# Performance work log

Hardware: AMD Instinct MI355X
Metric: run time of the kernel (lower is better)

Reference implementation:

```python
import jax, jax.numpy as jnp
import numpy as np

USER_COUNT = 100000
ITEM_COUNT = 50000
N_NODES = USER_COUNT + ITEM_COUNT
NNZ = 4800000
EMB = 64
BATCH = 4096


def setup_inputs() -> dict:
    key = jax.random.key(0)
    k1, k2, k3, k4, k5, k6, k7 = jax.random.split(key, 7)
    return {
        "user_emb": jax.random.normal(k1, (USER_COUNT, EMB), dtype=jnp.float32),
        "item_emb": jax.random.normal(k2, (ITEM_COUNT, EMB), dtype=jnp.float32),
        "adj_vals": jax.random.uniform(k3, (NNZ,), dtype=jnp.float32),
        "adj_row": jax.random.randint(k4, (NNZ,), 0, N_NODES, dtype=jnp.int64),
        "adj_col": jax.random.randint(k5, (NNZ,), 0, N_NODES, dtype=jnp.int64),
        "users": jax.random.randint(k6, (BATCH,), 0, USER_COUNT, dtype=jnp.int64),
        "items": jax.random.randint(k7, (BATCH,), 0, ITEM_COUNT, dtype=jnp.int64),
        "n_layers": 3,
    }


def _spmm(adj_row, adj_col, adj_vals, x):
    # sparse (N,N) @ dense (N,D): gather source rows, scale by edge values, scatter-add to dest
    msgs = adj_vals[:, None] * x[adj_col]  # [nnz, D]
    return jax.ops.segment_sum(msgs, adj_row, num_segments=N_NODES)


def reference(user_emb, item_emb, adj_vals, adj_row, adj_col, users, items, n_layers):
    ego = jnp.concatenate([user_emb, item_emb], axis=0)  # [N, D]
    for _ in range(n_layers):
        ego = _spmm(adj_row, adj_col, adj_vals, ego)
    user_all = ego[:USER_COUNT]
    item_all = ego[USER_COUNT:]
    return (user_all[users], item_all[items])
```

## Files before the change

### kernel.cpp

```cpp
#include <hip/hip_runtime.h>
#include <hip/hip_bf16.h>

#define USER_COUNT 100000
#define ITEM_COUNT 50000
#define N_NODES    150000
#define EMB        64
#define BATCH      4096

#define NFINE      586
#define FSHIFT     8
#define NBLK_P     512
#define PTHREADS   512

__device__ inline unsigned short f2bf_raw(float f) {
    __hip_bfloat16 h = __float2bfloat16(f);
    unsigned short u; __builtin_memcpy(&u, &h, 2); return u;
}

__global__ __launch_bounds__(PTHREADS) void count_kernel(
        const int* __restrict__ rows, int* __restrict__ counts, int nnz) {
    __shared__ int cnt[NFINE];
    const int b = blockIdx.x, t = threadIdx.x;
    for (int f = t; f < NFINE; f += PTHREADS) cnt[f] = 0;
    __syncthreads();
    const int per = (nnz + NBLK_P - 1) / NBLK_P;
    const int s = b * per, e = min(s + per, nnz);
    for (int i = s + t; i < e; i += PTHREADS)
        atomicAdd(&cnt[rows[i] >> FSHIFT], 1);
    __syncthreads();
    for (int f = t; f < NFINE; f += PTHREADS)
        counts[f * NBLK_P + b] = cnt[f];
}

__global__ __launch_bounds__(NBLK_P) void reduce_tot(
        const int* __restrict__ counts, int* __restrict__ tot) {
    __shared__ int red[NBLK_P];
    const int f = blockIdx.x, t = threadIdx.x;
    red[t] = counts[f * NBLK_P + t];
    __syncthreads();
    for (int o = NBLK_P / 2; o > 0; o >>= 1) {
        if (t < o) red[t] += red[t + o];
        __syncthreads();
    }
    if (t == 0) tot[f] = red[0];
}

__global__ void scan_fbase_kernel(const int* __restrict__ tot,
                                  int* __restrict__ fbase) {
    if (threadIdx.x == 0) {
        int acc = 0;
        for (int f = 0; f < NFINE; ++f) { fbase[f] = acc; acc += tot[f]; }
    }
}

__global__ __launch_bounds__(NBLK_P) void scan_offs(
        const int* __restrict__ counts, const int* __restrict__ fbase,
        int* __restrict__ offs) {
    __shared__ int s[NBLK_P];
    const int f = blockIdx.x, t = threadIdx.x;
    const int c = counts[f * NBLK_P + t];
    s[t] = c;
    __syncthreads();
    for (int o = 1; o < NBLK_P; o <<= 1) {
        int v = (t >= o) ? s[t - o] : 0;
        __syncthreads();
        s[t] += v;
        __syncthreads();
    }
    offs[f * NBLK_P + t] = fbase[f] + s[t] - c;
}

__global__ __launch_bounds__(PTHREADS) void partition_kernel(
        const float* __restrict__ vals,
        const int* __restrict__ rows,
        const int* __restrict__ cols,
        const int* __restrict__ offs,
        uint2* __restrict__ fine, int nnz) {
    __shared__ int cur[NFINE];
    const int b = blockIdx.x, t = threadIdx.x;
    for (int f = t; f < NFINE; f += PTHREADS) cur[f] = offs[f * NBLK_P + b];
    __syncthreads();
    const int per = (nnz + NBLK_P - 1) / NBLK_P;
    const int s = b * per, e = min(s + per, nnz);
    for (int i = s + t; i < e; i += PTHREADS) {
        int r = rows[i];
        int f = r >> FSHIFT;
        int pos = atomicAdd(&cur[f], 1);
        fine[pos] = make_uint2(__float_as_uint(vals[i]),
                               (unsigned)cols[i] | ((unsigned)(r & 255) << 18));
    }
}

__global__ __launch_bounds__(256) void bucket_sort_kernel(
        const uint2* __restrict__ fine,
        const int* __restrict__ tot,
        const int* __restrict__ fbase,
        float2* __restrict__ perm,
        int* __restrict__ row_ptr) {
    __shared__ int hist[256];
    __shared__ int off[256];
    __shared__ int cur[256];
    const int f   = blockIdx.x;
    const int tid = threadIdx.x;
    const int n   = tot[f];
    const int fb  = fbase[f];
    const uint2* src = fine + fb;

    hist[tid] = 0;
    __syncthreads();
    for (int k = tid; k < n; k += 256)
        atomicAdd(&hist[(src[k].y >> 18) & 255], 1);
    __syncthreads();
    if (tid == 0) {
        int acc = 0;
        for (int j = 0; j < 256; ++j) { off[j] = acc; acc += hist[j]; }
    }
    __syncthreads();
    cur[tid] = off[tid];
    int row = (f << FSHIFT) + tid;
    if (row <= N_NODES) row_ptr[row] = fb + off[tid];
    __syncthreads();
    for (int k = tid; k < n; k += 256) {
        uint2 e = src[k];
        int lrow = (e.y >> 18) & 255;
        int pos = fb + atomicAdd(&cur[lrow], 1);
        perm[pos] = make_float2(__uint_as_float(e.x),
                                __int_as_float((int)(e.y & 0x3FFFFu)));
    }
}

__global__ void to_bf16(const float4* __restrict__ ue,
                        const float4* __restrict__ ie,
                        uint2* __restrict__ xh) {
    int i = blockIdx.x * blockDim.x + threadIdx.x;
    const int n4 = (N_NODES * EMB) / 4;
    const int u4 = (USER_COUNT * EMB) / 4;
    if (i >= n4) return;
    float4 fv = (i < u4) ? ue[i] : ie[i - u4];
    uint2 o;
    o.x = (unsigned int)f2bf_raw(fv.x) | ((unsigned int)f2bf_raw(fv.y) << 16);
    o.y = (unsigned int)f2bf_raw(fv.z) | ((unsigned int)f2bf_raw(fv.w) << 16);
    xh[i] = o;
}

__global__ void spmm_bf16(const int* __restrict__ row_ptr,
                          const float2* __restrict__ perm,
                          const unsigned short* __restrict__ xh,
                          unsigned short* __restrict__ yh) {
    int wid  = (blockIdx.x * blockDim.x + threadIdx.x) >> 6;
    int lane = threadIdx.x & 63;
    int g    = lane >> 4;
    int s    = lane & 15;
    int r    = (wid << 2) + g;
    if (r >= N_NODES) return;

    int beg = row_ptr[r];
    int end = row_ptr[r + 1];

    const uint2* xv = (const uint2*)xh;
    float ax = 0.f, ay = 0.f, az = 0.f, aw = 0.f;

    int j = beg;
    for (; j + 3 < end; j += 4) {
        float2 e0 = perm[j];
        float2 e1 = perm[j + 1];
        float2 e2 = perm[j + 2];
        float2 e3 = perm[j + 3];
        uint2 u0 = xv[(((long long)__float_as_int(e0.y)) << 4) + s];
        uint2 u1 = xv[(((long long)__float_as_int(e1.y)) << 4) + s];
        uint2 u2 = xv[(((long long)__float_as_int(e2.y)) << 4) + s];
        uint2 u3 = xv[(((long long)__float_as_int(e3.y)) << 4) + s];
        ax += e0.x * __uint_as_float(u0.x << 16);
        ay += e0.x * __uint_as_float(u0.x & 0xffff0000u);
        az += e0.x * __uint_as_float(u0.y << 16);
        aw += e0.x * __uint_as_float(u0.y & 0xffff0000u);
        ax += e1.x * __uint_as_float(u1.x << 16);
        ay += e1.x * __uint_as_float(u1.x & 0xffff0000u);
        az += e1.x * __uint_as_float(u1.y << 16);
        aw += e1.x * __uint_as_float(u1.y & 0xffff0000u);
        ax += e2.x * __uint_as_float(u2.x << 16);
        ay += e2.x * __uint_as_float(u2.x & 0xffff0000u);
        az += e2.x * __uint_as_float(u2.y << 16);
        aw += e2.x * __uint_as_float(u2.y & 0xffff0000u);
        ax += e3.x * __uint_as_float(u3.x << 16);
        ay += e3.x * __uint_as_float(u3.x & 0xffff0000u);
        az += e3.x * __uint_as_float(u3.y << 16);
        aw += e3.x * __uint_as_float(u3.y & 0xffff0000u);
    }
    for (; j < end; ++j) {
        float2 e = perm[j];
        uint2 u = xv[(((long long)__float_as_int(e.y)) << 4) + s];
        ax += e.x * __uint_as_float(u.x << 16);
        ay += e.x * __uint_as_float(u.x & 0xffff0000u);
        az += e.x * __uint_as_float(u.y << 16);
        aw += e.x * __uint_as_float(u.y & 0xffff0000u);
    }

    uint2 o;
    o.x = (unsigned int)f2bf_raw(ax) | ((unsigned int)f2bf_raw(ay) << 16);
    o.y = (unsigned int)f2bf_raw(az) | ((unsigned int)f2bf_raw(aw) << 16);
    ((uint2*)yh)[(((long long)r) << 4) + s] = o;
}

__global__ void spmm_batch_kernel(const int* __restrict__ row_ptr,
                                  const float2* __restrict__ perm,
                                  const unsigned short* __restrict__ xh,
                                  const int* __restrict__ users,
                                  const int* __restrict__ items,
                                  float4* __restrict__ out) {
    int wid  = (blockIdx.x * blockDim.x + threadIdx.x) >> 6;
    int lane = threadIdx.x & 63;
    int g    = lane >> 4;
    int s    = lane & 15;
    int b    = (wid << 2) + g;
    if (b >= 2 * BATCH) return;
    int node = (b < BATCH) ? users[b] : (USER_COUNT + items[b - BATCH]);

    int beg = row_ptr[node];
    int end = row_ptr[node + 1];

    const uint2* xv = (const uint2*)xh;
    float ax = 0.f, ay = 0.f, az = 0.f, aw = 0.f;

    int j = beg;
    for (; j + 3 < end; j += 4) {
        float2 e0 = perm[j];
        float2 e1 = perm[j + 1];
        float2 e2 = perm[j + 2];
        float2 e3 = perm[j + 3];
        uint2 u0 = xv[(((long long)__float_as_int(e0.y)) << 4) + s];
        uint2 u1 = xv[(((long long)__float_as_int(e1.y)) << 4) + s];
        uint2 u2 = xv[(((long long)__float_as_int(e2.y)) << 4) + s];
        uint2 u3 = xv[(((long long)__float_as_int(e3.y)) << 4) + s];
        ax += e0.x * __uint_as_float(u0.x << 16);
        ay += e0.x * __uint_as_float(u0.x & 0xffff0000u);
        az += e0.x * __uint_as_float(u0.y << 16);
        aw += e0.x * __uint_as_float(u0.y & 0xffff0000u);
        ax += e1.x * __uint_as_float(u1.x << 16);
        ay += e1.x * __uint_as_float(u1.x & 0xffff0000u);
        az += e1.x * __uint_as_float(u1.y << 16);
        aw += e1.x * __uint_as_float(u1.y & 0xffff0000u);
        ax += e2.x * __uint_as_float(u2.x << 16);
        ay += e2.x * __uint_as_float(u2.x & 0xffff0000u);
        az += e2.x * __uint_as_float(u2.y << 16);
        aw += e2.x * __uint_as_float(u2.y & 0xffff0000u);
        ax += e3.x * __uint_as_float(u3.x << 16);
        ay += e3.x * __uint_as_float(u3.x & 0xffff0000u);
        az += e3.x * __uint_as_float(u3.y << 16);
        aw += e3.x * __uint_as_float(u3.y & 0xffff0000u);
    }
    for (; j < end; ++j) {
        float2 e = perm[j];
        uint2 u = xv[(((long long)__float_as_int(e.y)) << 4) + s];
        ax += e.x * __uint_as_float(u.x << 16);
        ay += e.x * __uint_as_float(u.x & 0xffff0000u);
        az += e.x * __uint_as_float(u.y << 16);
        aw += e.x * __uint_as_float(u.y & 0xffff0000u);
    }

    out[(size_t)b * 16 + s] = make_float4(ax, ay, az, aw);
}

extern "C" void kernel_launch(void* const* d_in, const int* in_sizes, int n_in,
                              void* d_out, int out_size, void* d_ws, size_t ws_size,
                              hipStream_t stream) {
    const float* user_emb = (const float*)d_in[0];
    const float* item_emb = (const float*)d_in[1];
    const float* adj_vals = (const float*)d_in[2];
    const int*   adj_row  = (const int*)d_in[3];
    const int*   adj_col  = (const int*)d_in[4];
    const int*   users    = (const int*)d_in[5];
    const int*   items    = (const int*)d_in[6];

    const int nnz = in_sizes[2];

    char* p = (char*)d_ws;
    uint2* fine = (uint2*)p;
    unsigned short* xh_a = (unsigned short*)p;
    unsigned short* xh_b = xh_a + (size_t)N_NODES * EMB;
    p += (size_t)nnz * sizeof(uint2);
    float2* perm = (float2*)p;
    p += (size_t)nnz * sizeof(float2);
    int* row_ptr = (int*)p;
    p += (size_t)(N_NODES + 16) * sizeof(int);
    int* counts = (int*)p;  p += (size_t)NFINE * NBLK_P * sizeof(int);
    int* offs   = (int*)p;  p += (size_t)NFINE * NBLK_P * sizeof(int);
    int* tot    = (int*)p;  p += (size_t)NFINE * sizeof(int);
    int* fbase  = (int*)p;

    count_kernel<<<NBLK_P, PTHREADS, 0, stream>>>(adj_row, counts, nnz);
    reduce_tot<<<NFINE, NBLK_P, 0, stream>>>(counts, tot);
    scan_fbase_kernel<<<1, 64, 0, stream>>>(tot, fbase);
    scan_offs<<<NFINE, NBLK_P, 0, stream>>>(counts, fbase, offs);
    partition_kernel<<<NBLK_P, PTHREADS, 0, stream>>>(adj_vals, adj_row, adj_col,
                                                      offs, fine, nnz);
    bucket_sort_kernel<<<NFINE, 256, 0, stream>>>(fine, tot, fbase, perm, row_ptr);

    const int n4 = (N_NODES * EMB) / 4;
    to_bf16<<<(n4 + 255) / 256, 256, 0, stream>>>((const float4*)user_emb,
                                                  (const float4*)item_emb,
                                                  (uint2*)xh_a);

    const int spmm_blocks = (N_NODES / 4 + 3) / 4;
    spmm_bf16<<<spmm_blocks, 256, 0, stream>>>(row_ptr, perm, xh_a, xh_b);
    spmm_bf16<<<spmm_blocks, 256, 0, stream>>>(row_ptr, perm, xh_b, xh_a);
    spmm_batch_kernel<<<(2 * BATCH / 4 + 3) / 4, 256, 0, stream>>>(
        row_ptr, perm, xh_a, users, items, (float4*)d_out);
}
```

Measured before the change: 504.7 us.

## Stage partition tiles in LDS and widen SpMM gathers to 16-byte loads

The partition kernel now works on fixed 6400-edge tiles. It counts and scans the buckets locally, scatters edges into a shared-memory buffer, then writes each bucket's run contiguously to global memory, replacing scattered global writes. The SpMM and batch kernels assign 8 lanes per row with uint4 loads instead of 16 lanes with uint2, so one wavefront handles 8 rows and issues fewer, wider gathers. The cost is a second pass over rows, a binary search per element, heavy LDS use per block, and more registers per lane.

```diff
diff --git a/kernel.cpp b/kernel.cpp
--- a/kernel.cpp
+++ b/kernel.cpp
@@ -9,36 +9,35 @@
 
 #define NFINE      586
 #define FSHIFT     8
-#define NBLK_P     512
-#define PTHREADS   512
+#define TILE_E     6400
+#define NBSTRIDE   768
 
 __device__ inline unsigned short f2bf_raw(float f) {
     __hip_bfloat16 h = __float2bfloat16(f);
     unsigned short u; __builtin_memcpy(&u, &h, 2); return u;
 }
 
-__global__ __launch_bounds__(PTHREADS) void count_kernel(
+__global__ __launch_bounds__(512) void count_kernel(
         const int* __restrict__ rows, int* __restrict__ counts, int nnz) {
     __shared__ int cnt[NFINE];
     const int b = blockIdx.x, t = threadIdx.x;
-    for (int f = t; f < NFINE; f += PTHREADS) cnt[f] = 0;
-    __syncthreads();
-    const int per = (nnz + NBLK_P - 1) / NBLK_P;
-    const int s = b * per, e = min(s + per, nnz);
-    for (int i = s + t; i < e; i += PTHREADS)
+    for (int f = t; f < NFINE; f += 512) cnt[f] = 0;
+    __syncthreads();
+    const int s = b * TILE_E, e = min(s + TILE_E, nnz);
+    for (int i = s + t; i < e; i += 512)
         atomicAdd(&cnt[rows[i] >> FSHIFT], 1);
     __syncthreads();
-    for (int f = t; f < NFINE; f += PTHREADS)
-        counts[f * NBLK_P + b] = cnt[f];
-}
-
-__global__ __launch_bounds__(NBLK_P) void reduce_tot(
-        const int* __restrict__ counts, int* __restrict__ tot) {
-    __shared__ int red[NBLK_P];
+    for (int f = t; f < NFINE; f += 512)
+        counts[f * NBSTRIDE + b] = cnt[f];
+}
+
+__global__ __launch_bounds__(1024) void reduce_tot(
+        const int* __restrict__ counts, int* __restrict__ tot, int nblk) {
+    __shared__ int red[1024];
     const int f = blockIdx.x, t = threadIdx.x;
-    red[t] = counts[f * NBLK_P + t];
-    __syncthreads();
-    for (int o = NBLK_P / 2; o > 0; o >>= 1) {
+    red[t] = (t < nblk) ? counts[f * NBSTRIDE + t] : 0;
+    __syncthreads();
+    for (int o = 512; o > 0; o >>= 1) {
         if (t < o) red[t] += red[t + o];
         __syncthreads();
     }
@@ -53,41 +52,78 @@
     }
 }
 
-__global__ __launch_bounds__(NBLK_P) void scan_offs(
+__global__ __launch_bounds__(1024) void scan_offs(
         const int* __restrict__ counts, const int* __restrict__ fbase,
-        int* __restrict__ offs) {
-    __shared__ int s[NBLK_P];
+        int* __restrict__ offs, int nblk) {
+    __shared__ int s[1024];
     const int f = blockIdx.x, t = threadIdx.x;
-    const int c = counts[f * NBLK_P + t];
+    const int c = (t < nblk) ? counts[f * NBSTRIDE + t] : 0;
     s[t] = c;
     __syncthreads();
-    for (int o = 1; o < NBLK_P; o <<= 1) {
+    for (int o = 1; o < 1024; o <<= 1) {
         int v = (t >= o) ? s[t - o] : 0;
         __syncthreads();
         s[t] += v;
         __syncthreads();
     }
-    offs[f * NBLK_P + t] = fbase[f] + s[t] - c;
-}
-
-__global__ __launch_bounds__(PTHREADS) void partition_kernel(
+    if (t < nblk) offs[f * NBSTRIDE + t] = fbase[f] + s[t] - c;
+}
+
+__global__ __launch_bounds__(512) void partition_kernel(
         const float* __restrict__ vals,
         const int* __restrict__ rows,
         const int* __restrict__ cols,
         const int* __restrict__ offs,
         uint2* __restrict__ fine, int nnz) {
-    __shared__ int cur[NFINE];
+    __shared__ uint2 buf[TILE_E];
+    __shared__ int   cnt[NFINE];
+    __shared__ int   sloff[NFINE + 1];
+    __shared__ int   gb[NFINE];
+    __shared__ int   sscan[512];
     const int b = blockIdx.x, t = threadIdx.x;
-    for (int f = t; f < NFINE; f += PTHREADS) cur[f] = offs[f * NBLK_P + b];
-    __syncthreads();
-    const int per = (nnz + NBLK_P - 1) / NBLK_P;
-    const int s = b * per, e = min(s + per, nnz);
-    for (int i = s + t; i < e; i += PTHREADS) {
+    const int sbeg = b * TILE_E, send = min(sbeg + TILE_E, nnz);
+    const int n = send - sbeg;
+
+    for (int f = t; f < NFINE; f += 512) {
+        cnt[f] = 0;
+        gb[f] = offs[f * NBSTRIDE + b];
+    }
+    __syncthreads();
+    for (int i = sbeg + t; i < send; i += 512)
+        atomicAdd(&cnt[rows[i] >> FSHIFT], 1);
+    __syncthreads();
+    int c0 = (2 * t < NFINE) ? cnt[2 * t] : 0;
+    int c1 = (2 * t + 1 < NFINE) ? cnt[2 * t + 1] : 0;
+    sscan[t] = c0 + c1;
+    __syncthreads();
+    for (int o = 1; o < 512; o <<= 1) {
+        int v = (t >= o) ? sscan[t - o] : 0;
+        __syncthreads();
+        sscan[t] += v;
+        __syncthreads();
+    }
+    int base = (t == 0) ? 0 : sscan[t - 1];
+    if (2 * t < NFINE) sloff[2 * t] = base;
+    if (2 * t + 1 < NFINE) sloff[2 * t + 1] = base + c0;
+    if (t == 511) sloff[NFINE] = sscan[511];
+    __syncthreads();
+    for (int f = t; f < NFINE; f += 512) cnt[f] = sloff[f];
+    __syncthreads();
+    for (int i = sbeg + t; i < send; i += 512) {
         int r = rows[i];
         int f = r >> FSHIFT;
-        int pos = atomicAdd(&cur[f], 1);
-        fine[pos] = make_uint2(__float_as_uint(vals[i]),
-                               (unsigned)cols[i] | ((unsigned)(r & 255) << 18));
+        int pos = atomicAdd(&cnt[f], 1);
+        buf[pos] = make_uint2(__float_as_uint(vals[i]),
+                              (unsigned)cols[i] | ((unsigned)(r & 255) << 18));
+    }
+    __syncthreads();
+    for (int idx = t; idx < n; idx += 512) {
+        int lo = 0, hi = NFINE;
+        while (hi - lo > 1) {
+            int mid = (lo + hi) >> 1;
+            if (sloff[mid] <= idx) lo = mid; else hi = mid;
+        }
+        fine[gb[lo] + (idx - sloff[lo])] = buf[idx];
     }
 }
 
@@ -143,22 +179,33 @@
     xh[i] = o;
 }
 
+#define ACC8(U, W)                                      \
+    a0 += (W) * __uint_as_float((U).x << 16);           \
+    a1 += (W) * __uint_as_float((U).x & 0xffff0000u);   \
+    a2 += (W) * __uint_as_float((U).y << 16);           \
+    a3 += (W) * __uint_as_float((U).y & 0xffff0000u);   \
+    a4 += (W) * __uint_as_float((U).z << 16);           \
+    a5 += (W) * __uint_as_float((U).z & 0xffff0000u);   \
+    a6 += (W) * __uint_as_float((U).w << 16);           \
+    a7 += (W) * __uint_as_float((U).w & 0xffff0000u);
+
 __global__ void spmm_bf16(const int* __restrict__ row_ptr,
                           const float2* __restrict__ perm,
                           const unsigned short* __restrict__ xh,
                           unsigned short* __restrict__ yh) {
     int wid  = (blockIdx.x * blockDim.x + threadIdx.x) >> 6;
     int lane = threadIdx.x & 63;
-    int g    = lane >> 4;
-    int s    = lane & 15;
-    int r    = (wid << 2) + g;
+    int g    = lane >> 3;
+    int s    = lane & 7;
+    int r    = (wid << 3) + g;
     if (r >= N_NODES) return;
 
     int beg = row_ptr[r];
     int end = row_ptr[r + 1];
 
-    const uint2* xv = (const uint2*)xh;
-    float ax = 0.f, ay = 0.f, az = 0.f, aw = 0.f;
+    const uint4* xv = (const uint4*)xh;
+    float a0 = 0.f, a1 = 0.f, a2 = 0.f, a3 = 0.f;
+    float a4 = 0.f, a5 = 0.f, a6 = 0.f, a7 = 0.f;
 
     int j = beg;
     for (; j + 3 < end; j += 4) {
@@ -166,40 +213,24 @@
         float2 e1 = perm[j + 1];
         float2 e2 = perm[j + 2];
         float2 e3 = perm[j + 3];
-        uint2 u0 = xv[(((long long)__float_as_int(e0.y)) << 4) + s];
-        uint2 u1 = xv[(((long long)__float_as_int(e1.y)) << 4) + s];
-        uint2 u2 = xv[(((long long)__float_as_int(e2.y)) << 4) + s];
-        uint2 u3 = xv[(((long long)__float_as_int(e3.y)) << 4) + s];
-        ax += e0.x * __uint_as_float(u0.x << 16);
-        ay += e0.x * __uint_as_float(u0.x & 0xffff0000u);
-        az += e0.x * __uint_as_float(u0.y << 16);
-        aw += e0.x * __uint_as_float(u0.y & 0xffff0000u);
-        ax += e1.x * __uint_as_float(u1.x << 16);
-        ay += e1.x * __uint_as_float(u1.x & 0xffff0000u);
-        az += e1.x * __uint_as_float(u1.y << 16);
-        aw += e1.x * __uint_as_float(u1.y & 0xffff0000u);
-        ax += e2.x * __uint_as_float(u2.x << 16);
-        ay += e2.x * __uint_as_float(u2.x & 0xffff0000u);
-        az += e2.x * __uint_as_float(u2.y << 16);
-        aw += e2.x * __uint_as_float(u2.y & 0xffff0000u);
-        ax += e3.x * __uint_as_float(u3.x << 16);
-        ay += e3.x * __uint_as_float(u3.x & 0xffff0000u);
-        az += e3.x * __uint_as_float(u3.y << 16);
-        aw += e3.x * __uint_as_float(u3.y & 0xffff0000u);
+        uint4 u0 = xv[(((long long)__float_as_int(e0.y)) << 3) + s];
+        uint4 u1 = xv[(((long long)__float_as_int(e1.y)) << 3) + s];
+        uint4 u2 = xv[(((long long)__float_as_int(e2.y)) << 3) + s];
+        uint4 u3 = xv[(((long long)__float_as_int(e3.y)) << 3) + s];
+        ACC8(u0, e0.x) ACC8(u1, e1.x) ACC8(u2, e2.x) ACC8(u3, e3.x)
     }
     for (; j < end; ++j) {
         float2 e = perm[j];
-        uint2 u = xv[(((long long)__float_as_int(e.y)) << 4) + s];
-        ax += e.x * __uint_as_float(u.x << 16);
-        ay += e.x * __uint_as_float(u.x & 0xffff0000u);
-        az += e.x * __uint_as_float(u.y << 16);
-        aw += e.x * __uint_as_float(u.y & 0xffff0000u);
-    }
-
-    uint2 o;
-    o.x = (unsigned int)f2bf_raw(ax) | ((unsigned int)f2bf_raw(ay) << 16);
-    o.y = (unsigned int)f2bf_raw(az) | ((unsigned int)f2bf_raw(aw) << 16);
-    ((uint2*)yh)[(((long long)r) << 4) + s] = o;
+        uint4 u = xv[(((long long)__float_as_int(e.y)) << 3) + s];
+        ACC8(u, e.x)
+    }
+
+    uint4 o;
+    o.x = (unsigned)f2bf_raw(a0) | ((unsigned)f2bf_raw(a1) << 16);
+    o.y = (unsigned)f2bf_raw(a2) | ((unsigned)f2bf_raw(a3) << 16);
+    o.z = (unsigned)f2bf_raw(a4) | ((unsigned)f2bf_raw(a5) << 16);
+    o.w = (unsigned)f2bf_raw(a6) | ((unsigned)f2bf_raw(a7) << 16);
+    ((uint4*)yh)[(((long long)r) << 3) + s] = o;
 }
 
 __global__ void spmm_batch_kernel(const int* __restrict__ row_ptr,
@@ -210,17 +241,18 @@
                                   float4* __restrict__ out) {
     int wid  = (blockIdx.x * blockDim.x + threadIdx.x) >> 6;
     int lane = threadIdx.x & 63;
-    int g    = lane >> 4;
-    int s    = lane & 15;
-    int b    = (wid << 2) + g;
+    int g    = lane >> 3;
+    int s    = lane & 7;
+    int b    = (wid << 3) + g;
     if (b >= 2 * BATCH) return;
     int node = (b < BATCH) ? users[b] : (USER_COUNT + items[b - BATCH]);
 
     int beg = row_ptr[node];
     int end = row_ptr[node + 1];
 
-    const uint2* xv = (const uint2*)xh;
-    float ax = 0.f, ay = 0.f, az = 0.f, aw = 0.f;
+    const uint4* xv = (const uint4*)xh;
+    float a0 = 0.f, a1 = 0.f, a2 = 0.f, a3 = 0.f;
+    float a4 = 0.f, a5 = 0.f, a6 = 0.f, a7 = 0.f;
 
     int j = beg;
     for (; j + 3 < end; j += 4) {
@@ -228,37 +260,20 @@
         float2 e1 = perm[j + 1];
         float2 e2 = perm[j + 2];
         float2 e3 = perm[j + 3];
-        uint2 u0 = xv[(((long long)__float_as_int(e0.y)) << 4) + s];
-        uint2 u1 = xv[(((long long)__float_as_int(e1.y)) << 4) + s];
-        uint2 u2 = xv[(((long long)__float_as_int(e2.y)) << 4) + s];
-        uint2 u3 = xv[(((long long)__float_as_int(e3.y)) << 4) + s];
-        ax += e0.x * __uint_as_float(u0.x << 16);
-        ay += e0.x * __uint_as_float(u0.x & 0xffff0000u);
-        az += e0.x * __uint_as_float(u0.y << 16);
-        aw += e0.x * __uint_as_float(u0.y & 0xffff0000u);
-        ax += e1.x * __uint_as_float(u1.x << 16);
-        ay += e1.x * __uint_as_float(u1.x & 0xffff0000u);
-        az += e1.x * __uint_as_float(u1.y << 16);
-        aw += e1.x * __uint_as_float(u1.y & 0xffff0000u);
-        ax += e2.x * __uint_as_float(u2.x << 16);
-        ay += e2.x * __uint_as_float(u2.x & 0xffff0000u);
-        az += e2.x * __uint_as_float(u2.y << 16);
-        aw += e2.x * __uint_as_float(u2.y & 0xffff0000u);
-        ax += e3.x * __uint_as_float(u3.x << 16);
-        ay += e3.x * __uint_as_float(u3.x & 0xffff0000u);
-        az += e3.x * __uint_as_float(u3.y << 16);
-        aw += e3.x * __uint_as_float(u3.y & 0xffff0000u);
+        uint4 u0 = xv[(((long long)__float_as_int(e0.y)) << 3) + s];
+        uint4 u1 = xv[(((long long)__float_as_int(e1.y)) << 3) + s];
+        uint4 u2 = xv[(((long long)__float_as_int(e2.y)) << 3) + s];
+        uint4 u3 = xv[(((long long)__float_as_int(e3.y)) << 3) + s];
+        ACC8(u0, e0.x) ACC8(u1, e1.x) ACC8(u2, e2.x) ACC8(u3, e3.x)
     }
     for (; j < end; ++j) {
         float2 e = perm[j];
-        uint2 u = xv[(((long long)__float_as_int(e.y)) << 4) + s];
-        ax += e.x * __uint_as_float(u.x << 16);
-        ay += e.x * __uint_as_float(u.x & 0xffff0000u);
-        az += e.x * __uint_as_float(u.y << 16);
-        aw += e.x * __uint_as_float(u.y & 0xffff0000u);
-    }
-
-    out[(size_t)b * 16 + s] = make_float4(ax, ay, az, aw);
+        uint4 u = xv[(((long long)__float_as_int(e.y)) << 3) + s];
+        ACC8(u, e.x)
+    }
+
+    out[(size_t)b * 16 + 2 * s]     = make_float4(a0, a1, a2, a3);
+    out[(size_t)b * 16 + 2 * s + 1] = make_float4(a4, a5, a6, a7);
 }
 
 extern "C" void kernel_launch(void* const* d_in, const int* in_sizes, int n_in,
@@ -272,7 +287,8 @@
     const int*   users    = (const int*)d_in[5];
     const int*   items    = (const int*)d_in[6];
 
-    const int nnz = in_sizes[2];
+    const int nnz  = in_sizes[2];
+    const int nblk = (nnz + TILE_E - 1) / TILE_E;
 
     char* p = (char*)d_ws;
     uint2* fine = (uint2*)p;
@@ -283,17 +299,17 @@
     p += (size_t)nnz * sizeof(float2);
     int* row_ptr = (int*)p;
     p += (size_t)(N_NODES + 16) * sizeof(int);
-    int* counts = (int*)p;  p += (size_t)NFINE * NBLK_P * sizeof(int);
-    int* offs   = (int*)p;  p += (size_t)NFINE * NBLK_P * sizeof(int);
+    int* counts = (int*)p;  p += (size_t)NFINE * NBSTRIDE * sizeof(int);
+    int* offs   = (int*)p;  p += (size_t)NFINE * NBSTRIDE * sizeof(int);
     int* tot    = (int*)p;  p += (size_t)NFINE * sizeof(int);
     int* fbase  = (int*)p;
 
-    count_kernel<<<NBLK_P, PTHREADS, 0, stream>>>(adj_row, counts, nnz);
-    reduce_tot<<<NFINE, NBLK_P, 0, stream>>>(counts, tot);
+    count_kernel<<<nblk, 512, 0, stream>>>(adj_row, counts, nnz);
+    reduce_tot<<<NFINE, 1024, 0, stream>>>(counts, tot, nblk);
     scan_fbase_kernel<<<1, 64, 0, stream>>>(tot, fbase);
-    scan_offs<<<NFINE, NBLK_P, 0, stream>>>(counts, fbase, offs);
-    partition_kernel<<<NBLK_P, PTHREADS, 0, stream>>>(adj_vals, adj_row, adj_col,
-                                                      offs, fine, nnz);
+    scan_offs<<<NFINE, 1024, 0, stream>>>(counts, fbase, offs, nblk);
+    partition_kernel<<<nblk, 512, 0, stream>>>(adj_vals, adj_row, adj_col,
+                                               offs, fine, nnz);
     bucket_sort_kernel<<<NFINE, 256, 0, stream>>>(fine, tot, fbase, perm, row_ptr);
 
     const int n4 = (N_NODES * EMB) / 4;
@@ -301,9 +317,9 @@
                                                   (const float4*)item_emb,
                                                   (uint2*)xh_a);
 
-    const int spmm_blocks = (N_NODES / 4 + 3) / 4;
+    const int spmm_blocks = (N_NODES / 8 + 3) / 4;
     spmm_bf16<<<spmm_blocks, 256, 0, stream>>>(row_ptr, perm, xh_a, xh_b);
     spmm_bf16<<<spmm_blocks, 256, 0, stream>>>(row_ptr, perm, xh_b, xh_a);
-    spmm_batch_kernel<<<(2 * BATCH / 4 + 3) / 4, 256, 0, stream>>>(
+    spmm_batch_kernel<<<(2 * BATCH / 8) / 4, 256, 0, stream>>>(
         row_ptr, perm, xh_a, users, items, (float4*)d_out);
 }
```

Measured after the change: 468.0 us. 7.3% less time.
